# Performance work log

Measured on AMD Instinct MI355X. Metric: run time of the kernel, lower is better.

The kernel has to match this reference:

```python
import jax, jax.numpy as jnp
import numpy as np

N_CELLS = 200_000
N_FACES = 400_000
N_POINTS = 200_000
E_CF = 800_000
E_FP = 800_000
E_PP = 1_200_000
IN_C, IN_F, HID, OUT = 8, 8, 64, 128


def setup_inputs() -> dict:
    key = jax.random.key(0)
    ks = jax.random.split(key, 18)
    return {
        "x_centers": jax.random.normal(ks[0], (N_CELLS, IN_C), jnp.float32),
        "x_face": jax.random.normal(ks[1], (N_FACES, IN_F), jnp.float32),
        "W_cf": jax.random.normal(ks[2], (IN_C, HID), jnp.float32) * 0.1,
        "b_cf": jax.random.normal(ks[3], (HID,), jnp.float32) * 0.1,
        "W_fp": jax.random.normal(ks[4], (HID + IN_F, OUT), jnp.float32) * 0.1,
        "b_fp": jax.random.normal(ks[5], (OUT,), jnp.float32) * 0.1,
        "W_pp": jax.random.normal(ks[6], (OUT, OUT), jnp.float32) * 0.1,
        "W_pp_root": jax.random.normal(ks[7], (OUT, OUT), jnp.float32) * 0.1,
        "b_pp": jax.random.normal(ks[8], (OUT,), jnp.float32) * 0.1,
        "ea_cf": jax.random.uniform(ks[9], (E_CF,), jnp.float32),
        "ea_fp": jax.random.uniform(ks[10], (E_FP,), jnp.float32),
        "ea_pp": jax.random.uniform(ks[11], (E_PP,), jnp.float32),
        "src_cf": jax.random.randint(ks[12], (E_CF,), 0, N_CELLS, jnp.int32),
        "dst_cf": jax.random.randint(ks[13], (E_CF,), 0, N_FACES, jnp.int32),
        "src_fp": jax.random.randint(ks[14], (E_FP,), 0, N_FACES, jnp.int32),
        "dst_fp": jax.random.randint(ks[15], (E_FP,), 0, N_POINTS, jnp.int32),
        "src_pp": jax.random.randint(ks[16], (E_PP,), 0, N_POINTS, jnp.int32),
        "dst_pp": jax.random.randint(ks[17], (E_PP,), 0, N_POINTS, jnp.int32),
    }


def _graph_conv(x, W, b, src, dst, ea, n_dst):
    # transform-then-gather (small in-dim GEMM first), weight by edge_attr, scatter-sum
    h = x @ W                                   # [n_src, out]
    msg = h[src] * ea[:, None]                  # [E, out]
    return jax.ops.segment_sum(msg, dst, num_segments=n_dst) + b


def reference(x_centers, x_face, W_cf, b_cf, W_fp, b_fp, W_pp, W_pp_root, b_pp,
              ea_cf, ea_fp, ea_pp, src_cf, dst_cf, src_fp, dst_fp, src_pp, dst_pp):
    # layerCenterFace: cells -> faces
    y_face = _graph_conv(x_centers, W_cf, b_cf, src_cf, dst_cf, ea_cf, N_FACES)
    # concat learned face features with raw face features
    x = jnp.concatenate([y_face, x_face], axis=-1)          # [N_FACES, 72]
    # layerFacePoint: faces -> points
    y_pt = _graph_conv(x, W_fp, b_fp, src_fp, dst_fp, ea_fp, N_POINTS)
    # layerPointPoint: points -> points with root/self term
    msg = (y_pt @ W_pp)[src_pp] * ea_pp[:, None]            # [E_PP, 128]
    agg = jax.ops.segment_sum(msg, dst_pp, num_segments=N_POINTS)
    return y_pt @ W_pp_root + agg + b_pp                    # [N_POINTS, 128]
```

## Files before the change

kernel.cpp:

```cpp
#include <hip/hip_runtime.h>
#include <hip/hip_bf16.h>

#define N_CELLS  200000
#define N_FACES  400000
#define N_POINTS 200000
#define E_CF     800000
#define E_FP     800000
#define E_PP     1200000
#define CAP_CF   16
#define CAP_FP   24
#define CAP_PP   32
#define OVF_CAP  4096
#define LDA128   136

typedef __attribute__((ext_vector_type(8))) short bf16x8;
typedef __attribute__((ext_vector_type(8))) unsigned short u16x8;
typedef __attribute__((ext_vector_type(4))) float f32x4;

__device__ __forceinline__ float bf2f(unsigned short u) {
    union { unsigned int i; float f; } v; v.i = ((unsigned int)u) << 16; return v.f;
}
__device__ __forceinline__ unsigned short f2bf(float f) {
    __hip_bfloat16 h = __float2bfloat16(f);
    return *reinterpret_cast<unsigned short*>(&h);
}
__device__ __forceinline__ int2 ldnt2(const int2* p) {
    long long v = __builtin_nontemporal_load((const long long*)p);
    int2 r; r.x = (int)(v & 0xffffffffLL); r.y = (int)(v >> 32); return r;
}

__device__ __forceinline__ void fill_fixed(const int* __restrict__ src,
                                           const int* __restrict__ dst,
                                           const float* __restrict__ ea,
                                           int nE, int rlo, int rhi, int cap,
                                           int tid0, int stride,
                                           int* __restrict__ cnt,
                                           int2* __restrict__ pe,
                                           int* __restrict__ ovfn,
                                           int4* __restrict__ ovf) {
    for (int e = tid0; e < nE; e += stride) {
        int4 d4 = *(const int4*)(dst + e);
        int4 s4 = *(const int4*)(src + e);
        float4 w4 = *(const float4*)(ea + e);
        int dd[4] = {d4.x, d4.y, d4.z, d4.w};
        int ss[4] = {s4.x, s4.y, s4.z, s4.w};
        float ww[4] = {w4.x, w4.y, w4.z, w4.w};
#pragma unroll
        for (int i = 0; i < 4; ++i) {
            int d = dd[i];
            if (d >= rlo && d < rhi) {
                int t = atomicAdd(&cnt[d], 1);
                if (t < cap)
                    pe[(size_t)d * cap + t] = make_int2(ss[i], __float_as_int(ww[i]));
                else {
                    int g = atomicAdd(ovfn, 1);
                    if (g < OVF_CAP) ovf[g] = make_int4(d, ss[i], __float_as_int(ww[i]), 0);
                }
            }
        }
    }
}

__global__ __launch_bounds__(256) void k_fillA(const int* __restrict__ src_cf,
                                               const int* __restrict__ dst_cf,
                                               const float* __restrict__ ea_cf,
                                               int* __restrict__ cnt_cf,
                                               int2* __restrict__ pe_cf,
                                               const int* __restrict__ src_fp,
                                               const int* __restrict__ dst_fp,
                                               const float* __restrict__ ea_fp,
                                               int* __restrict__ cnt_fp,
                                               int2* __restrict__ pe_fp,
                                               int* __restrict__ ovfn,
                                               int4* __restrict__ ovf_cf,
                                               int4* __restrict__ ovf_fp,
                                               const float* __restrict__ W_cf,
                                               const float* __restrict__ b_cf,
                                               const float* __restrict__ W_fp,
                                               const float* __restrict__ b_fp,
                                               const float* __restrict__ W_rt,
                                               const float* __restrict__ W_pp,
                                               float* __restrict__ Wt,
                                               unsigned short* __restrict__ Bp_fin) {
    __shared__ float WcfS[512];
    __shared__ float bcfS[64];
    int b = blockIdx.x;
    if (b < 512) {
        int p = b & 3;
        int blk = b >> 2;
        int rlo = p * 100000, rhi = rlo + 100000;
        int tid0 = (blk * 256 + (int)threadIdx.x) * 4;
        fill_fixed(src_cf, dst_cf, ea_cf, E_CF, rlo, rhi, CAP_CF,
                   tid0, 128 * 256 * 4, cnt_cf, pe_cf, ovfn, ovf_cf);
    } else if (b < 1024) {
        int bb = b - 512;
        int p = bb & 3;
        int blk = bb >> 2;
        int rlo = p * 50000, rhi = rlo + 50000;
        int tid0 = (blk * 256 + (int)threadIdx.x) * 4;
        fill_fixed(src_fp, dst_fp, ea_fp, E_FP, rlo, rhi, CAP_FP,
                   tid0, 128 * 256 * 4, cnt_fp, pe_fp, ovfn + 1, ovf_fp);
    } else if (b < 1152) {
        int t = (b - 1024) * 256 + threadIdx.x;
        int j = t & 7, lane = (t >> 3) & 63, ct = (t >> 9) & 7, ks = t >> 12;
        int k = ks * 32 + ((lane >> 4) & 3) * 8 + j;
        int col = ct * 16 + (lane & 15);
        float v = (k < 128) ? W_rt[k * 128 + col] : W_pp[(k - 128) * 128 + col];
        Bp_fin[t] = f2bf(v);
    } else {
        for (int i = threadIdx.x; i < 512; i += 256) WcfS[i] = W_cf[i];
        if (threadIdx.x < 64) bcfS[threadIdx.x] = b_cf[threadIdx.x];
        __syncthreads();
        int t = threadIdx.x;
        int j = t & 127;
        if (t < 128) {
            float accW[8] = {};
            float accb = 0.f;
            for (int m = 0; m < 64; ++m) {
                float wf = W_fp[m * 128 + j];
#pragma unroll
                for (int k = 0; k < 8; ++k) accW[k] += WcfS[k * 64 + m] * wf;
                accb += bcfS[m] * wf;
            }
#pragma unroll
            for (int k = 0; k < 8; ++k) Wt[k * 128 + j] = accW[k];
            Wt[16 * 128 + j] = accb;
        } else {
#pragma unroll
            for (int k = 0; k < 8; ++k) Wt[(8 + k) * 128 + j] = W_fp[(64 + k) * 128 + j];
            Wt[17 * 128 + j] = b_fp[j];
        }
    }
}

__global__ __launch_bounds__(256) void k_fillB(const int* __restrict__ src_pp,
                                               const int* __restrict__ dst_pp,
                                               const float* __restrict__ ea_pp,
                                               int* __restrict__ cnt_pp,
                                               int2* __restrict__ pe_pp,
                                               int* __restrict__ ovfn,
                                               int4* __restrict__ ovf_pp,
                                               const float* __restrict__ xc,
                                               const int* __restrict__ cnt_cf,
                                               const int2* __restrict__ pe_cf,
                                               const int* __restrict__ ovfn_cf,
                                               const int4* __restrict__ ovf_cf,
                                               const float* __restrict__ x_face,
                                               float* __restrict__ aggcx) {
    int b = blockIdx.x;
    if (b < 512) {
        int p = b & 3;
        int blk = b >> 2;
        int rlo = p * 50000, rhi = rlo + 50000;
        int tid0 = (blk * 256 + (int)threadIdx.x) * 4;
        fill_fixed(src_pp, dst_pp, ea_pp, E_PP, rlo, rhi, CAP_PP,
                   tid0, 128 * 256 * 4, cnt_pp, pe_pp, ovfn + 2, ovf_pp);
        return;
    }
    int r = (b - 512) * 256 + threadIdx.x;
    if (r >= N_FACES) return;
    int n = cnt_cf[r]; if (n > CAP_CF) n = CAP_CF;
    const int2* prow = pe_cf + (size_t)r * CAP_CF;
    float a[8] = {};
    int e = 0;
    for (; e + 1 < n; e += 2) {
        int2 q0 = prow[e], q1 = prow[e + 1];
        float w0 = __int_as_float(q0.y), w1 = __int_as_float(q1.y);
        const float* p0 = xc + (size_t)q0.x * 8;
        const float* p1 = xc + (size_t)q1.x * 8;
        float4 u0 = *(const float4*)p0, u1 = *(const float4*)(p0 + 4);
        float4 v0 = *(const float4*)p1, v1 = *(const float4*)(p1 + 4);
        a[0] += w0 * u0.x + w1 * v0.x; a[1] += w0 * u0.y + w1 * v0.y;
        a[2] += w0 * u0.z + w1 * v0.z; a[3] += w0 * u0.w + w1 * v0.w;
        a[4] += w0 * u1.x + w1 * v1.x; a[5] += w0 * u1.y + w1 * v1.y;
        a[6] += w0 * u1.z + w1 * v1.z; a[7] += w0 * u1.w + w1 * v1.w;
    }
    if (e < n) {
        int2 q0 = prow[e];
        float w0 = __int_as_float(q0.y);
        const float* p0 = xc + (size_t)q0.x * 8;
        float4 u0 = *(const float4*)p0, u1 = *(const float4*)(p0 + 4);
        a[0] += w0 * u0.x; a[1] += w0 * u0.y; a[2] += w0 * u0.z; a[3] += w0 * u0.w;
        a[4] += w0 * u1.x; a[5] += w0 * u1.y; a[6] += w0 * u1.z; a[7] += w0 * u1.w;
    }
    int no = *ovfn_cf;
    if (no > 0) {
        if (no > OVF_CAP) no = OVF_CAP;
        for (int i = 0; i < no; ++i) {
            int4 o = ovf_cf[i];
            if (o.x == r) {
                float w0 = __int_as_float(o.z);
                const float* p0 = xc + (size_t)o.y * 8;
#pragma unroll
                for (int k = 0; k < 8; ++k) a[k] += w0 * p0[k];
            }
        }
    }
    float4 xf0 = *(const float4*)(x_face + (size_t)r * 8);
    float4 xf1 = *(const float4*)(x_face + (size_t)r * 8 + 4);
    float4* o4 = (float4*)(aggcx + (size_t)r * 16);
    o4[0] = make_float4(a[0], a[1], a[2], a[3]);
    o4[1] = make_float4(a[4], a[5], a[6], a[7]);
    o4[2] = xf0;
    o4[3] = xf1;
}

__global__ __launch_bounds__(256) void k_g17(const float* __restrict__ aggcx,
                                             const int* __restrict__ cnt,
                                             const int2* __restrict__ pe,
                                             const int* __restrict__ ovfn,
                                             const int4* __restrict__ ovf,
                                             const float* __restrict__ Wt,
                                             unsigned short* __restrict__ y_ptb) {
    int row = blockIdx.x * 256 + threadIdx.x;
    if (row >= N_POINTS) return;
    int n = cnt[row]; if (n > CAP_FP) n = CAP_FP;
    const int2* prow = pe + (size_t)row * CAP_FP;
    float a[16] = {};
    float s = 0.f;
    int e = 0;
    for (; e + 1 < n; e += 2) {
        int2 q0 = ldnt2(prow + e);
        int2 q1 = ldnt2(prow + e + 1);
        float w0 = __int_as_float(q0.y), w1 = __int_as_float(q1.y);
        const float4* v0 = (const float4*)(aggcx + (size_t)q0.x * 16);
        const float4* v1 = (const float4*)(aggcx + (size_t)q1.x * 16);
#pragma unroll
        for (int j = 0; j < 4; ++j) {
            float4 u = v0[j], v = v1[j];
            a[4 * j + 0] += w0 * u.x + w1 * v.x;
            a[4 * j + 1] += w0 * u.y + w1 * v.y;
            a[4 * j + 2] += w0 * u.z + w1 * v.z;
            a[4 * j + 3] += w0 * u.w + w1 * v.w;
        }
        s += w0 + w1;
    }
    if (e < n) {
        int2 q0 = ldnt2(prow + e);
        float w0 = __int_as_float(q0.y);
        const float4* v0 = (const float4*)(aggcx + (size_t)q0.x * 16);
#pragma unroll
        for (int j = 0; j < 4; ++j) {
            float4 u = v0[j];
            a[4 * j + 0] += w0 * u.x; a[4 * j + 1] += w0 * u.y;
            a[4 * j + 2] += w0 * u.z; a[4 * j + 3] += w0 * u.w;
        }
        s += w0;
    }
    int no = *ovfn;
    if (no > 0) {
        if (no > OVF_CAP) no = OVF_CAP;
        for (int i = 0; i < no; ++i) {
            int4 o = ovf[i];
            if (o.x == row) {
                float w0 = __int_as_float(o.z);
                const float* v0 = aggcx + (size_t)o.y * 16;
#pragma unroll
                for (int k = 0; k < 16; ++k) a[k] += w0 * v0[k];
                s += w0;
            }
        }
    }
    unsigned short* orow = y_ptb + (size_t)row * 128;
    for (int jc = 0; jc < 128; jc += 16) {
        float acc2[16];
        const float4* bb = (const float4*)(Wt + 17 * 128 + jc);
#pragma unroll
        for (int j4 = 0; j4 < 4; ++j4) {
            float4 w4 = bb[j4];
            acc2[4 * j4 + 0] = w4.x; acc2[4 * j4 + 1] = w4.y;
            acc2[4 * j4 + 2] = w4.z; acc2[4 * j4 + 3] = w4.w;
        }
#pragma unroll
        for (int k = 0; k < 16; ++k) {
            float av = a[k];
            const float4* wr = (const float4*)(Wt + k * 128 + jc);
#pragma unroll
            for (int j4 = 0; j4 < 4; ++j4) {
                float4 w4 = wr[j4];
                acc2[4 * j4 + 0] += av * w4.x; acc2[4 * j4 + 1] += av * w4.y;
                acc2[4 * j4 + 2] += av * w4.z; acc2[4 * j4 + 3] += av * w4.w;
            }
        }
        {
            const float4* wr = (const float4*)(Wt + 16 * 128 + jc);
#pragma unroll
            for (int j4 = 0; j4 < 4; ++j4) {
                float4 w4 = wr[j4];
                acc2[4 * j4 + 0] += s * w4.x; acc2[4 * j4 + 1] += s * w4.y;
                acc2[4 * j4 + 2] += s * w4.z; acc2[4 * j4 + 3] += s * w4.w;
            }
        }
        u16x8 o0, o1;
#pragma unroll
        for (int i = 0; i < 8; ++i) { o0[i] = f2bf(acc2[i]); o1[i] = f2bf(acc2[8 + i]); }
        *(u16x8*)(orow + jc) = o0;
        *(u16x8*)(orow + jc + 8) = o1;
    }
}

__global__ __launch_bounds__(256) void k_gpp_fin(const unsigned short* __restrict__ feat,
                                                 const int* __restrict__ cnt,
                                                 const int2* __restrict__ pe,
                                                 const int* __restrict__ ovfn,
                                                 const int4* __restrict__ ovf,
                                                 const unsigned short* __restrict__ A1,
                                                 const unsigned short* __restrict__ Bp,
                                                 const float* __restrict__ bias,
                                                 float* __restrict__ out) {
    __shared__ __align__(16) unsigned short Asub[32 * LDA128];
    const int w = threadIdx.x >> 6;
    const int lane = threadIdx.x & 63;
    const int l = lane & 31;
    const int R0 = blockIdx.x * 32;
    for (int rr = 0; rr < 4; ++rr) {
        int row = R0 + w * 8 + rr * 2 + (lane >> 5);
        int n = cnt[row]; if (n > CAP_PP) n = CAP_PP;
        const int2* prow = pe + (size_t)row * CAP_PP;
        float a0 = 0.f, a1 = 0.f, a2 = 0.f, a3 = 0.f;
        int e = 0;
        for (; e + 3 < n; e += 4) {
            int2 q0 = ldnt2(prow + e),     q1 = ldnt2(prow + e + 1);
            int2 q2 = ldnt2(prow + e + 2), q3 = ldnt2(prow + e + 3);
            float w0 = __int_as_float(q0.y), w1 = __int_as_float(q1.y);
            float w2 = __int_as_float(q2.y), w3 = __int_as_float(q3.y);
            const unsigned short* f0 = feat + ((size_t)q0.x << 7) + l;
            const unsigned short* f1 = feat + ((size_t)q1.x << 7) + l;
            const unsigned short* f2 = feat + ((size_t)q2.x << 7) + l;
            const unsigned short* f3 = feat + ((size_t)q3.x << 7) + l;
            a0 += w0 * bf2f(f0[0])  + w1 * bf2f(f1[0])  + w2 * bf2f(f2[0])  + w3 * bf2f(f3[0]);
            a1 += w0 * bf2f(f0[32]) + w1 * bf2f(f1[32]) + w2 * bf2f(f2[32]) + w3 * bf2f(f3[32]);
            a2 += w0 * bf2f(f0[64]) + w1 * bf2f(f1[64]) + w2 * bf2f(f2[64]) + w3 * bf2f(f3[64]);
            a3 += w0 * bf2f(f0[96]) + w1 * bf2f(f1[96]) + w2 * bf2f(f2[96]) + w3 * bf2f(f3[96]);
        }
        for (; e < n; ++e) {
            int2 q0 = ldnt2(prow + e);
            float w0 = __int_as_float(q0.y);
            const unsigned short* f0 = feat + ((size_t)q0.x << 7) + l;
            a0 += w0 * bf2f(f0[0]);  a1 += w0 * bf2f(f0[32]);
            a2 += w0 * bf2f(f0[64]); a3 += w0 * bf2f(f0[96]);
        }
        int no = *ovfn;
        if (no > 0) {
            if (no > OVF_CAP) no = OVF_CAP;
            for (int i = 0; i < no; ++i) {
                int4 o = ovf[i];
                if (o.x == row) {
                    float w0 = __int_as_float(o.z);
                    const unsigned short* f0 = feat + ((size_t)o.y << 7) + l;
                    a0 += w0 * bf2f(f0[0]);  a1 += w0 * bf2f(f0[32]);
                    a2 += w0 * bf2f(f0[64]); a3 += w0 * bf2f(f0[96]);
                }
            }
        }
        int lr = row - R0;
        Asub[lr * LDA128 + l]      = f2bf(a0);
        Asub[lr * LDA128 + 32 + l] = f2bf(a1);
        Asub[lr * LDA128 + 64 + l] = f2bf(a2);
        Asub[lr * LDA128 + 96 + l] = f2bf(a3);
    }
    __syncthreads();
    const int rg = w >> 1, cg = w & 1;
    bf16x8 bfr[8][4];
#pragma unroll
    for (int ks = 0; ks < 8; ++ks)
#pragma unroll
        for (int c = 0; c < 4; ++c) {
            int ct = cg * 4 + c;
            bfr[ks][c] = *(const bf16x8*)(Bp + ((size_t)(ks * 8 + ct) * 64 + lane) * 8);
        }
    f32x4 acc[4] = {};
    const unsigned short* a1p = A1 + (size_t)(R0 + rg * 16 + (lane & 15)) * 128 + ((lane >> 4) * 8);
    const unsigned short* a2p = Asub + (rg * 16 + (lane & 15)) * LDA128 + ((lane >> 4) * 8);
#pragma unroll
    for (int ks = 0; ks < 4; ++ks) {
        bf16x8 af = *(const bf16x8*)(a1p + ks * 32);
#pragma unroll
        for (int c = 0; c < 4; ++c)
            acc[c] = __builtin_amdgcn_mfma_f32_16x16x32_bf16(af, bfr[ks][c], acc[c], 0, 0, 0);
    }
#pragma unroll
    for (int ks = 0; ks < 4; ++ks) {
        bf16x8 af = *(const bf16x8*)(a2p + ks * 32);
#pragma unroll
        for (int c = 0; c < 4; ++c)
            acc[c] = __builtin_amdgcn_mfma_f32_16x16x32_bf16(af, bfr[ks + 4][c], acc[c], 0, 0, 0);
    }
    const int row0 = R0 + rg * 16;
    const int rbase = row0 + (lane >> 4) * 4;
#pragma unroll
    for (int c = 0; c < 4; ++c) {
        int gcol = cg * 64 + c * 16 + (lane & 15);
        float bv = bias[gcol];
#pragma unroll
        for (int r = 0; r < 4; ++r)
            __builtin_nontemporal_store(acc[c][r] + bv,
                                        &out[(size_t)(rbase + r) * 128 + gcol]);
    }
}

extern "C" void kernel_launch(void* const* d_in, const int* in_sizes, int n_in,
                              void* d_out, int out_size, void* d_ws, size_t ws_size,
                              hipStream_t stream) {
    const float* x_centers = (const float*)d_in[0];
    const float* x_face    = (const float*)d_in[1];
    const float* W_cf      = (const float*)d_in[2];
    const float* b_cf      = (const float*)d_in[3];
    const float* W_fp      = (const float*)d_in[4];
    const float* b_fp      = (const float*)d_in[5];
    const float* W_pp      = (const float*)d_in[6];
    const float* W_rt      = (const float*)d_in[7];
    const float* b_pp      = (const float*)d_in[8];
    const float* ea_cf     = (const float*)d_in[9];
    const float* ea_fp     = (const float*)d_in[10];
    const float* ea_pp     = (const float*)d_in[11];
    const int* src_cf      = (const int*)d_in[12];
    const int* dst_cf      = (const int*)d_in[13];
    const int* src_fp      = (const int*)d_in[14];
    const int* dst_fp      = (const int*)d_in[15];
    const int* src_pp      = (const int*)d_in[16];
    const int* dst_pp      = (const int*)d_in[17];
    float* out = (float*)d_out;

    char* ws = (char*)d_ws;
    float* aggcx           = (float*)(ws + 0);
    unsigned short* y_ptb  = (unsigned short*)(ws + 28000000);
    float* Wt              = (float*)(ws + 80000000);
    int2* pe_fp            = (int2*)(ws + 81000000);
    int2* pe_cf            = (int2*)(ws + 120000000);
    int2* pe_pp            = (int2*)(ws + 172000000);
    int*  cnt_cf           = (int*)(ws + 280000000);
    int*  cnt_fp           = (int*)(ws + 281600000);
    int*  cnt_pp           = (int*)(ws + 282400000);
    int*  ovfn             = (int*)(ws + 283200000);
    int4* ovf_cf           = (int4*)(ws + 284000000);
    int4* ovf_fp           = (int4*)(ws + 284100000);
    int4* ovf_pp           = (int4*)(ws + 284200000);
    unsigned short* Bp_fin = (unsigned short*)(ws + 284400000);

    hipMemsetAsync(cnt_cf, 0, 3200016, stream);
    k_fillA<<<1153, 256, 0, stream>>>(src_cf, dst_cf, ea_cf, cnt_cf, pe_cf,
                                      src_fp, dst_fp, ea_fp, cnt_fp, pe_fp,
                                      ovfn, ovf_cf, ovf_fp,
                                      W_cf, b_cf, W_fp, b_fp, W_rt, W_pp,
                                      Wt, Bp_fin);
    k_fillB<<<512 + 1563, 256, 0, stream>>>(src_pp, dst_pp, ea_pp, cnt_pp, pe_pp,
                                            ovfn, ovf_pp,
                                            x_centers, cnt_cf, pe_cf, ovfn, ovf_cf,
                                            x_face, aggcx);
    k_g17<<<782, 256, 0, stream>>>(aggcx, cnt_fp, pe_fp, ovfn + 1, ovf_fp, Wt, y_ptb);
    k_gpp_fin<<<6250, 256, 0, stream>>>(y_ptb, cnt_pp, pe_pp, ovfn + 2, ovf_pp,
                                        y_ptb, Bp_fin, b_pp, out);
}
```

Baseline: 373.0 us.

## Split k_g17 rows across 16-lane groups with LDS-staged weights

```diff
diff --git a/kernel.cpp b/kernel.cpp
--- a/kernel.cpp
+++ b/kernel.cpp
@@ -212,39 +212,27 @@
                                              const int4* __restrict__ ovf,
                                              const float* __restrict__ Wt,
                                              unsigned short* __restrict__ y_ptb) {
-    int row = blockIdx.x * 256 + threadIdx.x;
-    if (row >= N_POINTS) return;
+    __shared__ float WtS[18 * 128];
+    for (int i = threadIdx.x; i < 18 * 128; i += 256) WtS[i] = Wt[i];
+    __syncthreads();
+    const int grp = threadIdx.x >> 4;
+    const int l = threadIdx.x & 15;
+    const int row = blockIdx.x * 16 + grp;
     int n = cnt[row]; if (n > CAP_FP) n = CAP_FP;
     const int2* prow = pe + (size_t)row * CAP_FP;
-    float a[16] = {};
-    float s = 0.f;
+    float acc = 0.f, s = 0.f;
     int e = 0;
     for (; e + 1 < n; e += 2) {
         int2 q0 = ldnt2(prow + e);
         int2 q1 = ldnt2(prow + e + 1);
         float w0 = __int_as_float(q0.y), w1 = __int_as_float(q1.y);
-        const float4* v0 = (const float4*)(aggcx + (size_t)q0.x * 16);
-        const float4* v1 = (const float4*)(aggcx + (size_t)q1.x * 16);
-#pragma unroll
-        for (int j = 0; j < 4; ++j) {
-            float4 u = v0[j], v = v1[j];
-            a[4 * j + 0] += w0 * u.x + w1 * v.x;
-            a[4 * j + 1] += w0 * u.y + w1 * v.y;
-            a[4 * j + 2] += w0 * u.z + w1 * v.z;
-            a[4 * j + 3] += w0 * u.w + w1 * v.w;
-        }
+        acc += w0 * aggcx[(size_t)q0.x * 16 + l] + w1 * aggcx[(size_t)q1.x * 16 + l];
         s += w0 + w1;
     }
     if (e < n) {
         int2 q0 = ldnt2(prow + e);
         float w0 = __int_as_float(q0.y);
-        const float4* v0 = (const float4*)(aggcx + (size_t)q0.x * 16);
-#pragma unroll
-        for (int j = 0; j < 4; ++j) {
-            float4 u = v0[j];
-            a[4 * j + 0] += w0 * u.x; a[4 * j + 1] += w0 * u.y;
-            a[4 * j + 2] += w0 * u.z; a[4 * j + 3] += w0 * u.w;
-        }
+        acc += w0 * aggcx[(size_t)q0.x * 16 + l];
         s += w0;
     }
     int no = *ovfn;
@@ -254,49 +242,34 @@
             int4 o = ovf[i];
             if (o.x == row) {
                 float w0 = __int_as_float(o.z);
-                const float* v0 = aggcx + (size_t)o.y * 16;
-#pragma unroll
-                for (int k = 0; k < 16; ++k) a[k] += w0 * v0[k];
+                acc += w0 * aggcx[(size_t)o.y * 16 + l];
                 s += w0;
             }
         }
     }
-    unsigned short* orow = y_ptb + (size_t)row * 128;
-    for (int jc = 0; jc < 128; jc += 16) {
-        float acc2[16];
-        const float4* bb = (const float4*)(Wt + 17 * 128 + jc);
-#pragma unroll
-        for (int j4 = 0; j4 < 4; ++j4) {
-            float4 w4 = bb[j4];
-            acc2[4 * j4 + 0] = w4.x; acc2[4 * j4 + 1] = w4.y;
-            acc2[4 * j4 + 2] = w4.z; acc2[4 * j4 + 3] = w4.w;
-        }
-#pragma unroll
-        for (int k = 0; k < 16; ++k) {
-            float av = a[k];
-            const float4* wr = (const float4*)(Wt + k * 128 + jc);
-#pragma unroll
-            for (int j4 = 0; j4 < 4; ++j4) {
-                float4 w4 = wr[j4];
-                acc2[4 * j4 + 0] += av * w4.x; acc2[4 * j4 + 1] += av * w4.y;
-                acc2[4 * j4 + 2] += av * w4.z; acc2[4 * j4 + 3] += av * w4.w;
-            }
-        }
-        {
-            const float4* wr = (const float4*)(Wt + 16 * 128 + jc);
-#pragma unroll
-            for (int j4 = 0; j4 < 4; ++j4) {
-                float4 w4 = wr[j4];
-                acc2[4 * j4 + 0] += s * w4.x; acc2[4 * j4 + 1] += s * w4.y;
-                acc2[4 * j4 + 2] += s * w4.z; acc2[4 * j4 + 3] += s * w4.w;
-            }
-        }
-        u16x8 o0, o1;
-#pragma unroll
-        for (int i = 0; i < 8; ++i) { o0[i] = f2bf(acc2[i]); o1[i] = f2bf(acc2[8 + i]); }
-        *(u16x8*)(orow + jc) = o0;
-        *(u16x8*)(orow + jc + 8) = o1;
-    }
+    const int jc = l * 8;
+    float a2[8];
+    {
+        const float4* bb = (const float4*)(WtS + 17 * 128 + jc);
+        const float4* ss4 = (const float4*)(WtS + 16 * 128 + jc);
+        float4 b0 = bb[0], b1 = bb[1], s0 = ss4[0], s1 = ss4[1];
+        a2[0] = b0.x + s * s0.x; a2[1] = b0.y + s * s0.y;
+        a2[2] = b0.z + s * s0.z; a2[3] = b0.w + s * s0.w;
+        a2[4] = b1.x + s * s1.x; a2[5] = b1.y + s * s1.y;
+        a2[6] = b1.z + s * s1.z; a2[7] = b1.w + s * s1.w;
+    }
+#pragma unroll
+    for (int k = 0; k < 16; ++k) {
+        float av = __shfl(acc, k, 16);
+        const float4* wr = (const float4*)(WtS + k * 128 + jc);
+        float4 w0 = wr[0], w1 = wr[1];
+        a2[0] += av * w0.x; a2[1] += av * w0.y; a2[2] += av * w0.z; a2[3] += av * w0.w;
+        a2[4] += av * w1.x; a2[5] += av * w1.y; a2[6] += av * w1.z; a2[7] += av * w1.w;
+    }
+    u16x8 o0;
+#pragma unroll
+    for (int i = 0; i < 8; ++i) o0[i] = f2bf(a2[i]);
+    *(u16x8*)(y_ptb + (size_t)row * 128 + jc) = o0;
 }
 
 __global__ __launch_bounds__(256) void k_gpp_fin(const unsigned short* __restrict__ feat,
@@ -448,7 +421,7 @@
                                             ovfn, ovf_pp,
                                             x_centers, cnt_cf, pe_cf, ovfn, ovf_cf,
                                             x_face, aggcx);
-    k_g17<<<782, 256, 0, stream>>>(aggcx, cnt_fp, pe_fp, ovfn + 1, ovf_fp, Wt, y_ptb);
+    k_g17<<<12500, 256, 0, stream>>>(aggcx, cnt_fp, pe_fp, ovfn + 1, ovf_fp, Wt, y_ptb);
     k_gpp_fin<<<6250, 256, 0, stream>>>(y_ptb, cnt_pp, pe_pp, ovfn + 2, ovf_pp,
                                         y_ptb, Bp_fin, b_pp, out);
 }
```

New measurement: 373.6 us. Within noise of the previous version (+0.2%).
